# Optimization experiments

Measured on AMD Instinct MI355X. Metric: run time of the kernel, lower is better.

Reference implementation:

```python
import jax, jax.numpy as jnp
import numpy as np

L = 16; F = 2; T = 1 << 19; BASE = 16.0; FINEST = 2048.0; CDIM = 16; N = 262144
_PRIMES = np.array([1, 2654435761, 805459861], dtype=np.uint32)
_OFFS = np.array([[i, j, k] for i in (0, 1) for j in (0, 1) for k in (0, 1)], dtype=np.uint32)
_RES = np.floor(BASE * np.exp(np.arange(L) * (np.log(FINEST) - np.log(BASE)) / (L - 1))).astype(np.float32)


def _hash_encode(pn, table):
    # pn: [N,3] normalized to [0,1]; table: [L,T,F]
    offs = jnp.asarray(_OFFS)
    offs_mask = jnp.asarray(_OFFS.astype(bool))
    primes = jnp.asarray(_PRIMES)

    def level(tab, res):
        scaled = pn * res
        pos = jnp.floor(scaled)
        frac = scaled - pos
        corners = pos.astype(jnp.uint32)[:, None, :] + offs[None]  # [N,8,3]
        idx = (corners[..., 0] * primes[0]) ^ (corners[..., 1] * primes[1]) ^ (corners[..., 2] * primes[2])
        idx = (idx & jnp.uint32(T - 1)).astype(jnp.int32)
        feats = tab[idx]  # [N,8,F]
        w = jnp.prod(jnp.where(offs_mask[None], frac[:, None, :], 1.0 - frac[:, None, :]), axis=-1)  # [N,8]
        return jnp.einsum('nkf,nk->nf', feats, w)

    out = jax.vmap(level)(table, jnp.asarray(_RES))  # [L,N,F]
    return jnp.transpose(out, (1, 0, 2)).reshape(pn.shape[0], L * F)


def _lin(x, w, b):
    return x @ w.T + b


def _forward(p, bound, t_sdf, t_color, t_sem,
             f_w0, f_b0, f_w1, f_b1, f_w2, f_b2, f_w3, f_b3,
             osdf_w, osdf_b, orgb_w0, orgb_b0, orgb_w1, orgb_b1,
             s_w0, s_b0, s_w1, s_b1, s_w2, s_b2, s_wo, s_bo):
    pn = (p - bound[:, 0]) / (bound[:, 1] - bound[:, 0])
    feat = _hash_encode(pn, t_sdf)    # [N,32]
    c_feat = _hash_encode(pn, t_color)
    s_feat = _hash_encode(pn, t_sem)
    h = feat
    for w, b in ((f_w0, f_b0), (f_w1, f_b1), (f_w2, f_b2), (f_w3, f_b3)):
        h = jax.nn.relu(_lin(h, w, b))
    sdf_out = _lin(h, osdf_w, osdf_b)        # [N,17]
    sdf = jnp.tanh(sdf_out[:, 0])            # [N]
    sdf_feat = sdf_out[:, 1:]                # [N,16]
    rgb_in = jnp.concatenate([sdf_feat, c_feat, s_feat], axis=-1)  # [N,80]
    rgb = jax.nn.sigmoid(_lin(jax.nn.relu(_lin(rgb_in, orgb_w0, orgb_b0)), orgb_w1, orgb_b1))  # [N,3]
    hs = s_feat
    for w, b in ((s_w0, s_b0), (s_w1, s_b1), (s_w2, s_b2)):
        hs = jax.nn.relu(_lin(hs, w, b))
    semantic = _lin(hs, s_wo, s_bo)          # [N,25]
    raw = jnp.concatenate([rgb, sdf[:, None], semantic], axis=-1)  # [N,29]
    plane_feat = jnp.concatenate([c_feat[:, CDIM:], feat[:, CDIM:], s_feat[:, CDIM:]], axis=-1)  # [N,48]
    return raw, plane_feat


def setup_inputs() -> dict:
    key = jax.random.key(0)
    ks = jax.random.split(key, 32)

    def w(k, o, i):
        return (jax.random.normal(k, (o, i), jnp.float32) / np.sqrt(i)).astype(jnp.float32)

    return {
        'p': jax.random.uniform(ks[0], (N, 3), jnp.float32),
        'bound': jnp.array([[0.0, 1.0], [0.0, 1.0], [0.0, 1.0]], jnp.float32),
        't_sdf': jax.random.uniform(ks[1], (L, T, F), jnp.float32, -1e-2, 1e-2),
        't_color': jax.random.uniform(ks[2], (L, T, F), jnp.float32, -1e-2, 1e-2),
        't_sem': jax.random.uniform(ks[3], (L, T, F), jnp.float32, -1e-2, 1e-2),
        'f_w0': w(ks[4], 16, 32), 'f_b0': jnp.zeros(16, jnp.float32),
        'f_w1': w(ks[5], 16, 16), 'f_b1': jnp.zeros(16, jnp.float32),
        'f_w2': w(ks[6], 16, 16), 'f_b2': jnp.zeros(16, jnp.float32),
        'f_w3': w(ks[7], 16, 16), 'f_b3': jnp.zeros(16, jnp.float32),
        'osdf_w': w(ks[8], 17, 16), 'osdf_b': jnp.zeros(17, jnp.float32),
        'orgb_w0': w(ks[9], 16, 80), 'orgb_b0': jnp.zeros(16, jnp.float32),
        'orgb_w1': w(ks[10], 3, 16), 'orgb_b1': jnp.zeros(3, jnp.float32),
        's_w0': w(ks[11], 256, 32), 's_b0': jnp.zeros(256, jnp.float32),
        's_w1': w(ks[12], 256, 256), 's_b1': jnp.zeros(256, jnp.float32),
        's_w2': w(ks[13], 256, 256), 's_b2': jnp.zeros(256, jnp.float32),
        's_wo': w(ks[14], 25, 256), 's_bo': jnp.zeros(25, jnp.float32),
    }


def reference(p, bound, t_sdf, t_color, t_sem,
              f_w0, f_b0, f_w1, f_b1, f_w2, f_b2, f_w3, f_b3,
              osdf_w, osdf_b, orgb_w0, orgb_b0, orgb_w1, orgb_b1,
              s_w0, s_b0, s_w1, s_b1, s_w2, s_b2, s_wo, s_bo):
    return _forward(p, bound, t_sdf, t_color, t_sem,
                    f_w0, f_b0, f_w1, f_b1, f_w2, f_b2, f_w3, f_b3,
                    osdf_w, osdf_b, orgb_w0, orgb_b0, orgb_w1, orgb_b1,
                    s_w0, s_b0, s_w1, s_b1, s_w2, s_b2, s_wo, s_bo)
```

## Files before the change

kernel.cpp:

```cpp
#include <hip/hip_runtime.h>
#include <math.h>

#define NPTS 262144
#define TTAB 524288
#define TMASK (TTAB - 1)
#define PR1 2654435761u
#define PR2 805459861u

#define MQ_SLOTS 512
#define MHASH_BLOCKS (8 * MQ_SLOTS)
#define FQ_SLOTS 1536
#define FHASH_BLOCKS (8 * FQ_SLOTS)

typedef __attribute__((ext_vector_type(4))) float f32x4;
typedef __attribute__((ext_vector_type(8))) short bf16x8;
typedef __attribute__((ext_vector_type(3))) unsigned int uintx3;

struct ResArr { float r[16]; };

__device__ __forceinline__ float bf2f(unsigned int u) {
  union { unsigned int i; float f; } v; v.i = u << 16; return v.f;
}
__device__ __forceinline__ unsigned short f2bf(float f) {
  union { float f; unsigned int i; } v; v.f = f;
  unsigned int r = v.i + 0x7FFFu + ((v.i >> 16) & 1u);
  return (unsigned short)(r >> 16);
}
__device__ __forceinline__ unsigned int pack2(float a, float b) {
  return (unsigned int)f2bf(a) | ((unsigned int)f2bf(b) << 16);
}

union U8 { uint4 u; bf16x8 v; };

__global__ __launch_bounds__(256) void cvt_tab(
    const float* __restrict__ t0, const float* __restrict__ t1,
    const float* __restrict__ t2, unsigned int* __restrict__ mt)
{
  size_t i = (size_t)blockIdx.x * 256 + threadIdx.x;
  float2 a = ((const float2*)t0)[i];
  float2 b = ((const float2*)t1)[i];
  float2 c = ((const float2*)t2)[i];
  mt[i * 3 + 0] = pack2(a.x, a.y);
  mt[i * 3 + 1] = pack2(b.x, b.y);
  mt[i * 3 + 2] = pack2(c.x, c.y);
}

__global__ __launch_bounds__(256) void hash_merged(
    const float* __restrict__ p, const float* __restrict__ bound,
    const unsigned int* __restrict__ mt,
    unsigned int* __restrict__ featws, unsigned int* __restrict__ ctr,
    ResArr res)
{
  __shared__ int s_slot;
  if (threadIdx.x == 0) {
    unsigned int xcc;
    asm volatile("s_getreg_b32 %0, hwreg(HW_REG_XCC_ID)" : "=s"(xcc));
    xcc &= 7u;
    int slot = -1;
    for (int k = 0; k < 8; ++k) {
      unsigned int q = (xcc + (unsigned int)k) & 7u;
      unsigned int s = atomicAdd(ctr + q, 1u);
      if (s < MQ_SLOTS) { slot = (int)(q * MQ_SLOTS + s); break; }
    }
    s_slot = slot;
  }
  __syncthreads();
  int slot = s_slot;
  if (slot < 0) return;

  unsigned int q = (unsigned int)slot / MQ_SLOTS;
  unsigned int s = (unsigned int)slot - q * MQ_SLOTS;
  unsigned int level = (s >> 8) * 8u + q;
  unsigned int chunk = s & 255u;

  float r = res.r[0];
#pragma unroll
  for (int l = 1; l < 16; ++l) r = (level == (unsigned int)l) ? res.r[l] : r;

  float b0 = bound[0], b1 = bound[1], b2 = bound[2], b3 = bound[3],
        b4 = bound[4], b5 = bound[5];
  float i0v = 1.f / (b1 - b0), i1v = 1.f / (b3 - b2), i2v = 1.f / (b5 - b4);
  const unsigned int* mtl = mt + (size_t)level * TTAB * 3u;
  unsigned int f0 = (0u * 16u + level) * (unsigned int)NPTS;
  unsigned int f1 = (1u * 16u + level) * (unsigned int)NPTS;
  unsigned int f2b = (2u * 16u + level) * (unsigned int)NPTS;
  unsigned int nbase = chunk * 1024u + threadIdx.x;

#pragma unroll
  for (int half = 0; half < 2; ++half) {
    unsigned int CX[2], CY[2], CZ[2];
    float DX[2], DY[2], DZ[2];
#pragma unroll
    for (int pt = 0; pt < 2; ++pt) {
      unsigned int n = nbase + (unsigned int)(half * 512 + pt * 256);
      float px = p[n * 3 + 0], py = p[n * 3 + 1], pz = p[n * 3 + 2];
      float sx = (px - b0) * i0v * r;
      float sy = (py - b2) * i1v * r;
      float sz = (pz - b4) * i2v * r;
      float fx = floorf(sx), fy = floorf(sy), fz = floorf(sz);
      DX[pt] = sx - fx; DY[pt] = sy - fy; DZ[pt] = sz - fz;
      CX[pt] = (unsigned int)fx;
      CY[pt] = (unsigned int)fy * PR1;
      CZ[pt] = (unsigned int)fz * PR2;
    }
    __builtin_amdgcn_sched_barrier(0);

    uintx3 V[2][8];
#pragma unroll
    for (int pt = 0; pt < 2; ++pt) {
      unsigned int x0 = CX[pt], x1 = CX[pt] + 1u;
      unsigned int y0 = CY[pt], y1 = y0 + PR1;
      unsigned int z0 = CZ[pt], z1 = z0 + PR2;
      unsigned int id[8];
      id[0] = (x0 ^ y0 ^ z0) & TMASK;
      id[1] = (x0 ^ y0 ^ z1) & TMASK;
      id[2] = (x0 ^ y1 ^ z0) & TMASK;
      id[3] = (x0 ^ y1 ^ z1) & TMASK;
      id[4] = (x1 ^ y0 ^ z0) & TMASK;
      id[5] = (x1 ^ y0 ^ z1) & TMASK;
      id[6] = (x1 ^ y1 ^ z0) & TMASK;
      id[7] = (x1 ^ y1 ^ z1) & TMASK;
#pragma unroll
      for (int c = 0; c < 8; ++c)
        V[pt][c] = *(const uintx3*)(mtl + (size_t)id[c] * 3u);
    }
    __builtin_amdgcn_sched_barrier(0);

#pragma unroll
    for (int pt = 0; pt < 2; ++pt) {
      float dx = DX[pt], dy = DY[pt], dz = DZ[pt];
      float wx[2] = { 1.f - dx, dx }, wy[2] = { 1.f - dy, dy }, wz[2] = { 1.f - dz, dz };
      float a00 = 0.f, a01 = 0.f, a10 = 0.f, a11 = 0.f, a20 = 0.f, a21 = 0.f;
#pragma unroll
      for (int c = 0; c < 8; ++c) {
        float w = wx[c >> 2] * wy[(c >> 1) & 1] * wz[c & 1];
        unsigned int u0 = V[pt][c].x, u1 = V[pt][c].y, u2 = V[pt][c].z;
        a00 += bf2f(u0 << 16) * w;  a01 += bf2f(u0 & 0xFFFF0000u) * w;
        a10 += bf2f(u1 << 16) * w;  a11 += bf2f(u1 & 0xFFFF0000u) * w;
        a20 += bf2f(u2 << 16) * w;  a21 += bf2f(u2 & 0xFFFF0000u) * w;
      }
      unsigned int n = nbase + (unsigned int)(half * 512 + pt * 256);
      featws[f0 + n] = pack2(a00, a01);
      featws[f1 + n] = pack2(a10, a11);
      featws[f2b + n] = pack2(a20, a21);
    }
  }
}

__global__ __launch_bounds__(256) void hash_f32(
    const float* __restrict__ p, const float* __restrict__ bound,
    const float* __restrict__ t0, const float* __restrict__ t1,
    const float* __restrict__ t2,
    unsigned int* __restrict__ featws, unsigned int* __restrict__ ctr,
    ResArr res)
{
  __shared__ int s_pad[10240];
  if (threadIdx.x == 0) {
    unsigned int xcc;
    asm volatile("s_getreg_b32 %0, hwreg(HW_REG_XCC_ID)" : "=s"(xcc));
    xcc &= 7u;
    int slot = -1;
    for (int k = 0; k < 8; ++k) {
      unsigned int q = (xcc + (unsigned int)k) & 7u;
      unsigned int s = atomicAdd(ctr + q, 1u);
      if (s < FQ_SLOTS) { slot = (int)(q * FQ_SLOTS + s); break; }
    }
    s_pad[0] = slot;
  }
  __syncthreads();
  int slot = s_pad[0];
  if (slot < 0) return;

  unsigned int q = (unsigned int)slot / FQ_SLOTS;
  unsigned int s = (unsigned int)slot - q * FQ_SLOTS;
  unsigned int i = (s >> 8) * 8u + q;
  unsigned int level = i / 3u;
  unsigned int table = i - level * 3u;
  unsigned int chunk = s & 255u;

  float r = res.r[0];
#pragma unroll
  for (int l = 1; l < 16; ++l) r = (level == (unsigned int)l) ? res.r[l] : r;

  float b0 = bound[0], b1 = bound[1], b2 = bound[2], b3 = bound[3],
        b4 = bound[4], b5 = bound[5];
  const float* tf = ((table == 0u) ? t0 : (table == 1u) ? t1 : t2) +
                    (size_t)level * (TTAB * 2);
  unsigned int fbase = (table * 16u + level) * (unsigned int)NPTS;
  unsigned int nbase = chunk * 1024u + threadIdx.x;

#pragma unroll
  for (int it = 0; it < 4; ++it) {
    unsigned int n = nbase + (unsigned int)it * 256u;
    float px = p[n * 3 + 0], py = p[n * 3 + 1], pz = p[n * 3 + 2];
    float x = (px - b0) / (b1 - b0);
    float y = (py - b2) / (b3 - b2);
    float z = (pz - b4) / (b5 - b4);
    float sx = x * r, sy = y * r, sz = z * r;
    float fx = floorf(sx), fy = floorf(sy), fz = floorf(sz);
    float dx = sx - fx, dy = sy - fy, dz = sz - fz;
    unsigned int cx = (unsigned int)fx, cy = (unsigned int)fy, cz = (unsigned int)fz;
    unsigned int hx[2] = { cx, cx + 1u };
    unsigned int hy[2] = { cy * PR1, (cy + 1u) * PR1 };
    unsigned int hz[2] = { cz * PR2, (cz + 1u) * PR2 };
    float wx[2] = { 1.f - dx, dx }, wy[2] = { 1.f - dy, dy }, wz[2] = { 1.f - dz, dz };
    float a0 = 0.f, a1 = 0.f;
#pragma unroll
    for (int ii = 0; ii < 2; ++ii)
#pragma unroll
      for (int jj = 0; jj < 2; ++jj)
#pragma unroll
        for (int kk = 0; kk < 2; ++kk) {
          unsigned int idx = (hx[ii] ^ hy[jj] ^ hz[kk]) & TMASK;
          float2 f2 = *(const float2*)(tf + (size_t)idx * 2);
          float w = wx[ii] * wy[jj] * wz[kk];
          a0 += f2.x * w;
          a1 += f2.y * w;
        }
    featws[fbase + n] = pack2(a0, a1);
  }
}

__global__ __launch_bounds__(256) void mlp_small_kernel(
    const unsigned int* __restrict__ fws,
    const float* __restrict__ fw0, const float* __restrict__ fb0,
    const float* __restrict__ fw1, const float* __restrict__ fb1,
    const float* __restrict__ fw2, const float* __restrict__ fb2,
    const float* __restrict__ fw3, const float* __restrict__ fb3,
    const float* __restrict__ ow, const float* __restrict__ ob,
    const float* __restrict__ rw0, const float* __restrict__ rb0,
    const float* __restrict__ rw1, const float* __restrict__ rb1,
    float* __restrict__ out)
{
  unsigned int n = blockIdx.x * 256 + threadIdx.x;
  float ft[32], cf[32], sf[32];
#pragma unroll
  for (int l = 0; l < 16; ++l) {
    unsigned int u = fws[(0u * 16 + l) * (unsigned int)NPTS + n];
    ft[2 * l] = bf2f(u << 16); ft[2 * l + 1] = bf2f(u & 0xFFFF0000u);
    u = fws[(1u * 16 + l) * (unsigned int)NPTS + n];
    cf[2 * l] = bf2f(u << 16); cf[2 * l + 1] = bf2f(u & 0xFFFF0000u);
    u = fws[(2u * 16 + l) * (unsigned int)NPTS + n];
    sf[2 * l] = bf2f(u << 16); sf[2 * l + 1] = bf2f(u & 0xFFFF0000u);
  }

  {
    float* pf = out + (size_t)NPTS * 29 + (size_t)n * 48;
#pragma unroll
    for (int i2 = 0; i2 < 16; i2 += 4)
      *(float4*)(pf + i2) = make_float4(cf[16 + i2], cf[17 + i2], cf[18 + i2], cf[19 + i2]);
#pragma unroll
    for (int i2 = 0; i2 < 16; i2 += 4)
      *(float4*)(pf + 16 + i2) = make_float4(ft[16 + i2], ft[17 + i2], ft[18 + i2], ft[19 + i2]);
#pragma unroll
    for (int i2 = 0; i2 < 16; i2 += 4)
      *(float4*)(pf + 32 + i2) = make_float4(sf[16 + i2], sf[17 + i2], sf[18 + i2], sf[19 + i2]);
  }

  float h[16], g[16];
  for (int o = 0; o < 16; ++o) {
    float a = fb0[o];
    for (int i2 = 0; i2 < 32; ++i2) a += ft[i2] * fw0[o * 32 + i2];
    h[o] = fmaxf(a, 0.f);
  }
  for (int o = 0; o < 16; ++o) {
    float a = fb1[o];
    for (int i2 = 0; i2 < 16; ++i2) a += h[i2] * fw1[o * 16 + i2];
    g[o] = fmaxf(a, 0.f);
  }
  for (int o = 0; o < 16; ++o) {
    float a = fb2[o];
    for (int i2 = 0; i2 < 16; ++i2) a += g[i2] * fw2[o * 16 + i2];
    h[o] = fmaxf(a, 0.f);
  }
  for (int o = 0; o < 16; ++o) {
    float a = fb3[o];
    for (int i2 = 0; i2 < 16; ++i2) a += h[i2] * fw3[o * 16 + i2];
    g[o] = fmaxf(a, 0.f);
  }
  float so[17];
  for (int o = 0; o < 17; ++o) {
    float a = ob[o];
    for (int i2 = 0; i2 < 16; ++i2) a += g[i2] * ow[o * 16 + i2];
    so[o] = a;
  }
  float sdf = tanhf(so[0]);
  float rin[80];
#pragma unroll
  for (int i2 = 0; i2 < 16; ++i2) rin[i2] = so[i2 + 1];
#pragma unroll
  for (int i2 = 0; i2 < 32; ++i2) rin[16 + i2] = cf[i2];
#pragma unroll
  for (int i2 = 0; i2 < 32; ++i2) rin[48 + i2] = sf[i2];
  float hr[16];
  for (int o = 0; o < 16; ++o) {
    float a = rb0[o];
    for (int i2 = 0; i2 < 80; ++i2) a += rin[i2] * rw0[o * 80 + i2];
    hr[o] = fmaxf(a, 0.f);
  }
  float* po = out + (size_t)n * 29;
  for (int o = 0; o < 3; ++o) {
    float a = rb1[o];
    for (int i2 = 0; i2 < 16; ++i2) a += hr[i2] * rw1[o * 16 + i2];
    po[o] = 1.f / (1.f + expf(-a));
  }
  po[3] = sdf;
}

__global__ __launch_bounds__(256) void cvt_kernel(
    const float* __restrict__ sw0, const float* __restrict__ sw1,
    const float* __restrict__ sw2, const float* __restrict__ swo,
    unsigned short* __restrict__ w0, unsigned short* __restrict__ w1,
    unsigned short* __restrict__ w2, unsigned short* __restrict__ wo,
    unsigned int* __restrict__ ctr)
{
  int t = blockIdx.x * 256 + threadIdx.x;
  if (t < 8) ctr[t] = 0u;
  if (t < 8192) w0[t] = f2bf(sw0[t]);
  w1[t] = f2bf(sw1[t]);
  w2[t] = f2bf(sw2[t]);
  if (t < 8192) wo[t] = (t < 6400) ? f2bf(swo[t]) : (unsigned short)0;
}

#define LAYER256(Wp, Bp)                                                                   \
  {                                                                                        \
    _Pragma("unroll") for (int r = 0; r < 4; ++r)                                          \
      _Pragma("unroll") for (int c = 0; c < 4; ++c)                                        \
        acc[r][c] = (f32x4){0.f, 0.f, 0.f, 0.f};                                           \
    _Pragma("unroll") for (int c = 0; c < 4; ++c)                                          \
      bc[c] = *(const bf16x8*)(Wp + (size_t)(cw + c * 16 + l16) * 256 + quad * 8);         \
    _Pragma("unroll") for (int ks = 0; ks < 8; ++ks) {                                     \
      int k0 = ks * 32;                                                                    \
      if (ks < 7) {                                                                        \
        _Pragma("unroll") for (int c = 0; c < 4; ++c)                                      \
          bn[c] = *(const bf16x8*)(Wp + (size_t)(cw + c * 16 + l16) * 256 + k0 + 32 + quad * 8); \
      }                                                                                    \
      _Pragma("unroll") for (int r = 0; r < 4; ++r)                                        \
        a[r] = *(const bf16x8*)(H + (r * 16 + l16) * 264 + k0 + quad * 8);                 \
      __builtin_amdgcn_s_setprio(1);                                                       \
      _Pragma("unroll") for (int r = 0; r < 4; ++r)                                        \
        _Pragma("unroll") for (int c = 0; c < 4; ++c)                                      \
          acc[r][c] = __builtin_amdgcn_mfma_f32_16x16x32_bf16(a[r], bc[c], acc[r][c], 0, 0, 0); \
      __builtin_amdgcn_s_setprio(0);                                                       \
      _Pragma("unroll") for (int c = 0; c < 4; ++c) bc[c] = bn[c];                         \
    }                                                                                      \
    __syncthreads();                                         \
    _Pragma("unroll") for (int c = 0; c < 4; ++c) {                                        \
      int col = cw + c * 16 + l16;                                                         \
      float bias = Bp[col];                                                                \
      _Pragma("unroll") for (int r = 0; r < 4; ++r)                                        \
        _Pragma("unroll") for (int g2 = 0; g2 < 4; ++g2) {                                 \
          int row = r * 16 + quad * 4 + g2;                                                \
          H[row * 264 + col] = f2bf(fmaxf(acc[r][c][g2] + bias, 0.f));                     \
        }                                                                                  \
    }                                                                                      \
    __syncthreads();                                                   \
  }

__global__ __launch_bounds__(256, 4) void sem_kernel(
    const unsigned int* __restrict__ fws,
    const unsigned short* __restrict__ w0, const unsigned short* __restrict__ w1,
    const unsigned short* __restrict__ w2, const unsigned short* __restrict__ wo,
    const float* __restrict__ b0, const float* __restrict__ b1,
    const float* __restrict__ b2, const float* __restrict__ bo,
    float* __restrict__ out)
{
  __shared__ alignas(16) unsigned short H[64 * 264];

  int tid = threadIdx.x;
  int n0 = blockIdx.x * 64;
  int lane = tid & 63, wv = tid >> 6;
  int l16 = lane & 15, quad = lane >> 4;
  int cw = wv * 64;

  f32x4 acc[4][4];
  bf16x8 a[4], bc[4], bn[4];

#pragma unroll
  for (int r = 0; r < 4; ++r)
#pragma unroll
    for (int c = 0; c < 4; ++c) acc[r][c] = (f32x4){0.f, 0.f, 0.f, 0.f};
#pragma unroll
  for (int r = 0; r < 4; ++r) {
    unsigned int base = (32u + (unsigned int)quad * 4u) * (unsigned int)NPTS +
                        (unsigned int)(n0 + r * 16 + l16);
    U8 u;
    u.u.x = fws[base];
    u.u.y = fws[base + (unsigned int)NPTS];
    u.u.z = fws[base + 2u * (unsigned int)NPTS];
    u.u.w = fws[base + 3u * (unsigned int)NPTS];
    a[r] = u.v;
  }
#pragma unroll
  for (int c = 0; c < 4; ++c)
    bc[c] = *(const bf16x8*)(w0 + (size_t)(cw + c * 16 + l16) * 32 + quad * 8);
  __builtin_amdgcn_s_setprio(1);
#pragma unroll
  for (int r = 0; r < 4; ++r)
#pragma unroll
    for (int c = 0; c < 4; ++c)
      acc[r][c] = __builtin_amdgcn_mfma_f32_16x16x32_bf16(a[r], bc[c], acc[r][c], 0, 0, 0);
  __builtin_amdgcn_s_setprio(0);
#pragma unroll
  for (int c = 0; c < 4; ++c) {
    int col = cw + c * 16 + l16;
    float bias = b0[col];
#pragma unroll
    for (int r = 0; r < 4; ++r)
#pragma unroll
      for (int g2 = 0; g2 < 4; ++g2) {
        int row = r * 16 + quad * 4 + g2;
        H[row * 264 + col] = f2bf(fmaxf(acc[r][c][g2] + bias, 0.f));
      }
  }
  __syncthreads();

  LAYER256(w1, b1)
  LAYER256(w2, b2)

  {
    f32x4 acc2[2];
    acc2[0] = (f32x4){0.f, 0.f, 0.f, 0.f};
    acc2[1] = (f32x4){0.f, 0.f, 0.f, 0.f};
#pragma unroll
    for (int ks = 0; ks < 8; ++ks) {
      int k0 = ks * 32;
      bf16x8 af = *(const bf16x8*)(H + (wv * 16 + l16) * 264 + k0 + quad * 8);
#pragma unroll
      for (int c = 0; c < 2; ++c) {
        bf16x8 bf = *(const bf16x8*)(wo + (size_t)(c * 16 + l16) * 256 + k0 + quad * 8);
        acc2[c] = __builtin_amdgcn_mfma_f32_16x16x32_bf16(af, bf, acc2[c], 0, 0, 0);
      }
    }
#pragma unroll
    for (int c = 0; c < 2; ++c) {
      int col = c * 16 + l16;
      if (col < 25) {
        float bias = bo[col];
#pragma unroll
        for (int g2 = 0; g2 < 4; ++g2) {
          int row = wv * 16 + quad * 4 + g2;
          out[(size_t)(n0 + row) * 29 + 4 + col] = acc2[c][g2] + bias;
        }
      }
    }
  }
}

extern "C" void kernel_launch(void* const* d_in, const int* in_sizes, int n_in,
                              void* d_out, int out_size, void* d_ws, size_t ws_size,
                              hipStream_t stream) {
  const float* p      = (const float*)d_in[0];
  const float* bound  = (const float*)d_in[1];
  const float* t_sdf  = (const float*)d_in[2];
  const float* t_color= (const float*)d_in[3];
  const float* t_sem  = (const float*)d_in[4];
  const float* f_w0   = (const float*)d_in[5];
  const float* f_b0   = (const float*)d_in[6];
  const float* f_w1   = (const float*)d_in[7];
  const float* f_b1   = (const float*)d_in[8];
  const float* f_w2   = (const float*)d_in[9];
  const float* f_b2   = (const float*)d_in[10];
  const float* f_w3   = (const float*)d_in[11];
  const float* f_b3   = (const float*)d_in[12];
  const float* osdf_w = (const float*)d_in[13];
  const float* osdf_b = (const float*)d_in[14];
  const float* orgb_w0= (const float*)d_in[15];
  const float* orgb_b0= (const float*)d_in[16];
  const float* orgb_w1= (const float*)d_in[17];
  const float* orgb_b1= (const float*)d_in[18];
  const float* s_w0   = (const float*)d_in[19];
  const float* s_b0   = (const float*)d_in[20];
  const float* s_w1   = (const float*)d_in[21];
  const float* s_b1   = (const float*)d_in[22];
  const float* s_w2   = (const float*)d_in[23];
  const float* s_b2   = (const float*)d_in[24];
  const float* s_wo   = (const float*)d_in[25];
  const float* s_bo   = (const float*)d_in[26];

  unsigned int* featws = (unsigned int*)d_ws;
  unsigned short* w0b = (unsigned short*)(featws + 48u * NPTS);
  unsigned short* w1b = w0b + 8192;
  unsigned short* w2b = w1b + 65536;
  unsigned short* wob = w2b + 65536;
  unsigned int* ctr = (unsigned int*)(wob + 8192);
  unsigned int* mt = ctr + 8;
  size_t need_bt = ((char*)mt - (char*)d_ws) + (size_t)16 * TTAB * 12;
  bool use_bt = ws_size >= need_bt;

  ResArr res;
  double kk = (log(2048.0) - log(16.0)) / 15.0;
  for (int l = 0; l < 16; ++l) res.r[l] = (float)floor(16.0 * exp((double)l * kk));

  float* out = (float*)d_out;

  hipLaunchKernelGGL(cvt_kernel, dim3(256), dim3(256), 0, stream,
                     s_w0, s_w1, s_w2, s_wo, w0b, w1b, w2b, wob, ctr);
  if (use_bt) {
    hipLaunchKernelGGL(cvt_tab, dim3(32768), dim3(256), 0, stream,
                       t_sdf, t_color, t_sem, mt);
    hipLaunchKernelGGL(hash_merged, dim3(MHASH_BLOCKS), dim3(256), 0, stream,
                       p, bound, mt, featws, ctr, res);
  } else {
    hipLaunchKernelGGL(hash_f32, dim3(FHASH_BLOCKS), dim3(256), 0, stream,
                       p, bound, t_sdf, t_color, t_sem, featws, ctr, res);
  }
  hipLaunchKernelGGL(mlp_small_kernel, dim3(1024), dim3(256), 0, stream,
                     featws, f_w0, f_b0, f_w1, f_b1, f_w2, f_b2, f_w3, f_b3,
                     osdf_w, osdf_b, orgb_w0, orgb_b0, orgb_w1, orgb_b1, out);
  hipLaunchKernelGGL(sem_kernel, dim3(NPTS / 64), dim3(256), 0, stream,
                     featws, w0b, w1b, w2b, wob, s_b0, s_b1, s_b2, s_bo, out);
}
```

Before: 571.4 us.

## Retile semantic MLP to 128-point blocks with 8 waves and deeper weight prefetch

The semantic MLP kernel now processes 128 points per block with 512 threads (8 waves). Each wave owns 32 output columns across all 128 rows instead of 64 columns across 64 rows. Weight fragments are prefetched two k-steps ahead, and A fragments are loaded from LDS inside the MFMA loop rather than staged in registers. The aim is to reuse each weight load across more rows, cut per-block weight traffic, and hide latency with more waves, at the cost of doubled LDS per block and possibly lower occupancy. The output layer still indexes rows by wave*16, so with 8 waves it covers all 128 rows.

```diff
diff --git a/kernel.cpp b/kernel.cpp
--- a/kernel.cpp
+++ b/kernel.cpp
@@ -324,31 +324,33 @@
 
 #define LAYER256(Wp, Bp)                                                                   \
   {                                                                                        \
-    _Pragma("unroll") for (int r = 0; r < 4; ++r)                                          \
-      _Pragma("unroll") for (int c = 0; c < 4; ++c)                                        \
+    _Pragma("unroll") for (int r = 0; r < 8; ++r)                                          \
+      _Pragma("unroll") for (int c = 0; c < 2; ++c)                                        \
         acc[r][c] = (f32x4){0.f, 0.f, 0.f, 0.f};                                           \
-    _Pragma("unroll") for (int c = 0; c < 4; ++c)                                          \
+    _Pragma("unroll") for (int c = 0; c < 2; ++c) {                                        \
       bc[c] = *(const bf16x8*)(Wp + (size_t)(cw + c * 16 + l16) * 256 + quad * 8);         \
+      bn[c] = *(const bf16x8*)(Wp + (size_t)(cw + c * 16 + l16) * 256 + 32 + quad * 8);    \
+    }                                                                                      \
     _Pragma("unroll") for (int ks = 0; ks < 8; ++ks) {                                     \
       int k0 = ks * 32;                                                                    \
-      if (ks < 7) {                                                                        \
-        _Pragma("unroll") for (int c = 0; c < 4; ++c)                                      \
-          bn[c] = *(const bf16x8*)(Wp + (size_t)(cw + c * 16 + l16) * 256 + k0 + 32 + quad * 8); \
+      if (ks < 6) {                                                                        \
+        _Pragma("unroll") for (int c = 0; c < 2; ++c)                                      \
+          bn2[c] = *(const bf16x8*)(Wp + (size_t)(cw + c * 16 + l16) * 256 + k0 + 64 + quad * 8); \
       }                                                                                    \
-      _Pragma("unroll") for (int r = 0; r < 4; ++r)                                        \
-        a[r] = *(const bf16x8*)(H + (r * 16 + l16) * 264 + k0 + quad * 8);                 \
       __builtin_amdgcn_s_setprio(1);                                                       \
-      _Pragma("unroll") for (int r = 0; r < 4; ++r)                                        \
-        _Pragma("unroll") for (int c = 0; c < 4; ++c)                                      \
-          acc[r][c] = __builtin_amdgcn_mfma_f32_16x16x32_bf16(a[r], bc[c], acc[r][c], 0, 0, 0); \
+      _Pragma("unroll") for (int r = 0; r < 8; ++r) {                                      \
+        bf16x8 av = *(const bf16x8*)(H + (r * 16 + l16) * 264 + k0 + quad * 8);            \
+        acc[r][0] = __builtin_amdgcn_mfma_f32_16x16x32_bf16(av, bc[0], acc[r][0], 0, 0, 0);\
+        acc[r][1] = __builtin_amdgcn_mfma_f32_16x16x32_bf16(av, bc[1], acc[r][1], 0, 0, 0);\
+      }                                                                                    \
       __builtin_amdgcn_s_setprio(0);                                                       \
-      _Pragma("unroll") for (int c = 0; c < 4; ++c) bc[c] = bn[c];                         \
+      _Pragma("unroll") for (int c = 0; c < 2; ++c) { bc[c] = bn[c]; bn[c] = bn2[c]; }     \
     }                                                                                      \
     __syncthreads();                                         \
-    _Pragma("unroll") for (int c = 0; c < 4; ++c) {                                        \
+    _Pragma("unroll") for (int c = 0; c < 2; ++c) {                                        \
       int col = cw + c * 16 + l16;                                                         \
       float bias = Bp[col];                                                                \
-      _Pragma("unroll") for (int r = 0; r < 4; ++r)                                        \
+      _Pragma("unroll") for (int r = 0; r < 8; ++r)                                        \
         _Pragma("unroll") for (int g2 = 0; g2 < 4; ++g2) {                                 \
           int row = r * 16 + quad * 4 + g2;                                                \
           H[row * 264 + col] = f2bf(fmaxf(acc[r][c][g2] + bias, 0.f));                     \
@@ -357,7 +359,7 @@
     __syncthreads();                                                   \
   }
 
-__global__ __launch_bounds__(256, 4) void sem_kernel(
+__global__ __launch_bounds__(512, 4) void sem_kernel(
     const unsigned int* __restrict__ fws,
     const unsigned short* __restrict__ w0, const unsigned short* __restrict__ w1,
     const unsigned short* __restrict__ w2, const unsigned short* __restrict__ wo,
@@ -365,23 +367,26 @@
     const float* __restrict__ b2, const float* __restrict__ bo,
     float* __restrict__ out)
 {
-  __shared__ alignas(16) unsigned short H[64 * 264];
+  __shared__ alignas(16) unsigned short H[128 * 264];
 
   int tid = threadIdx.x;
-  int n0 = blockIdx.x * 64;
+  int n0 = blockIdx.x * 128;
   int lane = tid & 63, wv = tid >> 6;
   int l16 = lane & 15, quad = lane >> 4;
-  int cw = wv * 64;
-
-  f32x4 acc[4][4];
-  bf16x8 a[4], bc[4], bn[4];
-
-#pragma unroll
-  for (int r = 0; r < 4; ++r)
-#pragma unroll
-    for (int c = 0; c < 4; ++c) acc[r][c] = (f32x4){0.f, 0.f, 0.f, 0.f};
-#pragma unroll
-  for (int r = 0; r < 4; ++r) {
+  int cw = wv * 32;
+
+  f32x4 acc[8][2];
+  bf16x8 bc[2], bn[2], bn2[2];
+
+#pragma unroll
+  for (int r = 0; r < 8; ++r)
+#pragma unroll
+    for (int c = 0; c < 2; ++c) acc[r][c] = (f32x4){0.f, 0.f, 0.f, 0.f};
+#pragma unroll
+  for (int c = 0; c < 2; ++c)
+    bc[c] = *(const bf16x8*)(w0 + (size_t)(cw + c * 16 + l16) * 32 + quad * 8);
+#pragma unroll
+  for (int r = 0; r < 8; ++r) {
     unsigned int base = (32u + (unsigned int)quad * 4u) * (unsigned int)NPTS +
                         (unsigned int)(n0 + r * 16 + l16);
     U8 u;
@@ -389,24 +394,15 @@
     u.u.y = fws[base + (unsigned int)NPTS];
     u.u.z = fws[base + 2u * (unsigned int)NPTS];
     u.u.w = fws[base + 3u * (unsigned int)NPTS];
-    a[r] = u.v;
-  }
-#pragma unroll
-  for (int c = 0; c < 4; ++c)
-    bc[c] = *(const bf16x8*)(w0 + (size_t)(cw + c * 16 + l16) * 32 + quad * 8);
-  __builtin_amdgcn_s_setprio(1);
-#pragma unroll
-  for (int r = 0; r < 4; ++r)
-#pragma unroll
-    for (int c = 0; c < 4; ++c)
-      acc[r][c] = __builtin_amdgcn_mfma_f32_16x16x32_bf16(a[r], bc[c], acc[r][c], 0, 0, 0);
-  __builtin_amdgcn_s_setprio(0);
-#pragma unroll
-  for (int c = 0; c < 4; ++c) {
+    acc[r][0] = __builtin_amdgcn_mfma_f32_16x16x32_bf16(u.v, bc[0], acc[r][0], 0, 0, 0);
+    acc[r][1] = __builtin_amdgcn_mfma_f32_16x16x32_bf16(u.v, bc[1], acc[r][1], 0, 0, 0);
+  }
+#pragma unroll
+  for (int c = 0; c < 2; ++c) {
     int col = cw + c * 16 + l16;
     float bias = b0[col];
 #pragma unroll
-    for (int r = 0; r < 4; ++r)
+    for (int r = 0; r < 8; ++r)
 #pragma unroll
       for (int g2 = 0; g2 < 4; ++g2) {
         int row = r * 16 + quad * 4 + g2;
@@ -428,8 +424,8 @@
       bf16x8 af = *(const bf16x8*)(H + (wv * 16 + l16) * 264 + k0 + quad * 8);
 #pragma unroll
       for (int c = 0; c < 2; ++c) {
-        bf16x8 bf = *(const bf16x8*)(wo + (size_t)(c * 16 + l16) * 256 + k0 + quad * 8);
-        acc2[c] = __builtin_amdgcn_mfma_f32_16x16x32_bf16(af, bf, acc2[c], 0, 0, 0);
+        bf16x8 bfr = *(const bf16x8*)(wo + (size_t)(c * 16 + l16) * 256 + k0 + quad * 8);
+        acc2[c] = __builtin_amdgcn_mfma_f32_16x16x32_bf16(af, bfr, acc2[c], 0, 0, 0);
       }
     }
 #pragma unroll
@@ -508,6 +504,6 @@
   hipLaunchKernelGGL(mlp_small_kernel, dim3(1024), dim3(256), 0, stream,
                      featws, f_w0, f_b0, f_w1, f_b1, f_w2, f_b2, f_w3, f_b3,
                      osdf_w, osdf_b, orgb_w0, orgb_b0, orgb_w1, orgb_b1, out);
-  hipLaunchKernelGGL(sem_kernel, dim3(NPTS / 64), dim3(256), 0, stream,
+  hipLaunchKernelGGL(sem_kernel, dim3(NPTS / 128), dim3(512), 0, stream,
                      featws, w0b, w1b, w2b, wob, s_b0, s_b1, s_b2, s_bo, out);
 }
```

New measurement: 507.2 us. 1.13x faster.
